# Kernel tuning notes

Measured on AMD Instinct MI355X. Metric: run time of the kernel, lower is better.

The kernel has to match this reference:

```python
import jax, jax.numpy as jnp
import numpy as np

N_HEADS = 16
MASK_FILL = -2.0**15 + 1.0  # -32767, matches torch reference


def setup_inputs() -> dict:
    key = jax.random.key(0)
    ks = jax.random.split(key, 10)
    B, N, D = 4, 2048, 1024
    sc = 0.02
    return {
        "q": jax.random.normal(ks[0], (B, N, D), jnp.float32),
        "k": jax.random.normal(ks[1], (B, N, D), jnp.float32),
        "v": jax.random.normal(ks[2], (B, N, D), jnp.float32),
        "Wq": jax.random.normal(ks[3], (D, D), jnp.float32) * sc,
        "bq": jnp.zeros((D,), jnp.float32),
        "Wk": jax.random.normal(ks[4], (D, D), jnp.float32) * sc,
        "bk": jnp.zeros((D,), jnp.float32),
        "Wv": jax.random.normal(ks[5], (D, D), jnp.float32) * sc,
        "bv": jnp.zeros((D,), jnp.float32),
        "Wo": jax.random.normal(ks[6], (D, D), jnp.float32) * sc,
    }


def reference(q, k, v, Wq, bq, Wk, bk, Wv, bv, Wo):
    B, N, D = q.shape
    H = N_HEADS
    dh = D // H
    scale = dh ** (-0.5)

    def proj(x, W, b):
        # torch nn.Linear: x @ W.T + b, W stored as (out, in)
        y = jnp.einsum('bnd,od->bno', x, W) + b
        return y.reshape(B, N, H, dh).transpose(0, 2, 1, 3)  # b h n d

    qh = proj(q, Wq, bq)
    kh = proj(k, Wk, bk)
    vh = proj(v, Wv, bv)

    scores = jnp.einsum('bhnd,bhmd->bhnm', qh, kh) * scale  # [B,H,N,N]
    causal = jnp.tril(jnp.ones((N, N), dtype=bool))
    scores = jnp.where(causal, scores, jnp.float32(MASK_FILL))
    attn = jax.nn.softmax(scores, axis=-1)
    x = jnp.einsum('bhnm,bhmd->bhnd', attn, vh)
    x = x.transpose(0, 2, 1, 3).reshape(B, N, D)  # b n (h d)
    return jnp.einsum('bnd,od->bno', x, Wo)  # to_out Linear, bias=False; dropout p=0
```

## Files before the change

### kernel.cpp

```cpp
#include <hip/hip_runtime.h>
#include <hip/hip_bf16.h>
#include <cstdint>
#include <cstddef>

typedef __bf16 bf16_t;
typedef __bf16 bf16x4 __attribute__((ext_vector_type(4)));
typedef __bf16 bf16x8 __attribute__((ext_vector_type(8)));
typedef float  f32x4  __attribute__((ext_vector_type(4)));

static constexpr int Bsz  = 4;
static constexpr int Nseq = 2048;
static constexpr int Dmod = 1024;
static constexpr int H    = 16;
static constexpr int DH   = 64;
static constexpr int M_TOT = Bsz * Nseq;
static constexpr int K    = 1024;
static constexpr int BM = 128, BN = 128, BK = 32;

#define WAITVM(N) asm volatile("s_waitcnt vmcnt(" #N ")" ::: "memory")

__device__ __forceinline__ f32x4 mfma16(bf16x8 a, bf16x8 b, f32x4 c) {
  return __builtin_amdgcn_mfma_f32_16x16x32_bf16(a, b, c, 0, 0, 0);
}

__device__ __forceinline__ bf16x8 cvt8(const float* p) {
  f32x4 lo = *(const f32x4*)(p);
  f32x4 hi = *(const f32x4*)(p + 4);
  bf16x8 r;
#pragma unroll
  for (int i = 0; i < 4; ++i) { r[i] = (bf16_t)lo[i]; r[4 + i] = (bf16_t)hi[i]; }
  return r;
}

__device__ __forceinline__ void async16(const bf16_t* g, bf16_t* l) {
  __builtin_amdgcn_global_load_lds(
      (const __attribute__((address_space(1))) void*)g,
      (__attribute__((address_space(3))) void*)l, 16, 0, 0);
}

struct CvtArgs {
  const float* src[7];
  bf16_t* dst[7];
  int n[7];
};

__global__ __launch_bounds__(256) void cvt_kernel(CvtArgs a) {
  const int z = blockIdx.y;
  const float* s = a.src[z];
  bf16x8* d = (bf16x8*)a.dst[z];
  const int n8 = a.n[z] >> 3;
  const int stride = gridDim.x * 256;
  for (int i = blockIdx.x * 256 + threadIdx.x; i < n8; i += stride)
    d[i] = cvt8(s + (size_t)i * 8);
}

template <int MODE, typename CT>
__device__ __forceinline__ void gemm_body(
    bf16_t (*As)[BM][BK], bf16_t (*Ws)[BN][BK],
    const bf16_t* __restrict__ A, const bf16_t* __restrict__ W,
    const float* __restrict__ bias, CT* __restrict__ C, float oscale) {
  const int tid  = threadIdx.x;
  const int lane = tid & 63;
  const int wave = tid >> 6;
  const int wm = wave & 1, wn = wave >> 1;
  const int row = lane & 15, quad = lane >> 4;

  const int m_blk = blockIdx.x * BM;
  const int n_blk = blockIdx.y * BN;

  f32x4 acc[4][4];
#pragma unroll
  for (int i = 0; i < 4; ++i)
#pragma unroll
    for (int j = 0; j < 4; ++j) acc[i][j] = (f32x4){0.f, 0.f, 0.f, 0.f};

  const int srow = lane >> 2;
  const int scol = (lane & 3) * 8;

  const bf16_t* Abase = A + (size_t)m_blk * K + scol;
  const bf16_t* Wbase = W + (size_t)n_blk * K + scol;

  constexpr int NT = K / BK;

  auto stage = [&](int t, int buf) {
#pragma unroll
    for (int j = 0; j < 2; ++j) {
      const int seg = wave * 2 + j;
      async16(Abase + (size_t)(seg * 16 + srow) * K + t * BK,
              &As[buf][seg * 16][0]);
      async16(Wbase + (size_t)(seg * 16 + srow) * K + t * BK,
              &Ws[buf][seg * 16][0]);
    }
  };

  stage(0, 0);
  stage(1, 1);
  int buf = 0, bufn = 2;

#pragma unroll 1
  for (int it = 0; it < NT; ++it) {
    if (it + 1 < NT) { WAITVM(4); } else { WAITVM(0); }
    __builtin_amdgcn_s_barrier();

    bf16x8 af[4], wf[4];
#pragma unroll
    for (int i = 0; i < 4; ++i)
      af[i] = *(const bf16x8*)(&As[buf][wm * 64 + i * 16 + row][quad * 8]);
#pragma unroll
    for (int i = 0; i < 4; ++i)
      wf[i] = *(const bf16x8*)(&Ws[buf][wn * 64 + i * 16 + row][quad * 8]);

    if (it + 2 < NT) stage(it + 2, bufn);

#pragma unroll
    for (int i = 0; i < 4; ++i)
#pragma unroll
      for (int j = 0; j < 4; ++j) {
        if (MODE == 1)
          acc[i][j] = mfma16(af[i], wf[j], acc[i][j]);
        else
          acc[i][j] = mfma16(wf[j], af[i], acc[i][j]);
      }

    buf  = (buf  == 2) ? 0 : buf  + 1;
    bufn = (bufn == 2) ? 0 : bufn + 1;
  }

  if (MODE == 0) {
#pragma unroll
    for (int i = 0; i < 4; ++i) {
      const int m = m_blk + wm * 64 + i * 16 + row;
      const int b = m >> 11, n = m & 2047;
#pragma unroll
      for (int j = 0; j < 4; ++j) {
        const int o0 = n_blk + wn * 64 + j * 16 + quad * 4;
        const int hh = o0 >> 6, od = o0 & 63;
        const f32x4 bv4 = *(const f32x4*)(bias + o0);
        const size_t idx0 = (((size_t)b * H + hh) * Nseq + n) * DH + od;
        bf16x4 pkt;
#pragma unroll
        for (int r = 0; r < 4; ++r)
          pkt[r] = (bf16_t)((acc[i][j][r] + bv4[r]) * oscale);
        *(bf16x4*)((bf16_t*)C + idx0) = pkt;
      }
    }
  } else if (MODE == 2) {
#pragma unroll
    for (int i = 0; i < 4; ++i) {
      const int m = m_blk + wm * 64 + i * 16 + row;
#pragma unroll
      for (int j = 0; j < 4; ++j) {
        const int o0 = n_blk + wn * 64 + j * 16 + quad * 4;
        *(f32x4*)((float*)C + (size_t)m * Dmod + o0) = acc[i][j];
      }
    }
  } else {
#pragma unroll
    for (int j = 0; j < 4; ++j) {
      const int o = n_blk + wn * 64 + j * 16 + row;
      const float bv = bias[o];
      const int hh = o >> 6, od = o & 63;
#pragma unroll
      for (int i = 0; i < 4; ++i) {
        const int m0 = m_blk + wm * 64 + i * 16 + quad * 4;
        const int b = m0 >> 11, n = m0 & 2047;
        const size_t idx0 = (((size_t)b * H + hh) * DH + od) * Nseq + n;
        bf16x4 pkt;
#pragma unroll
        for (int r = 0; r < 4; ++r)
          pkt[r] = (bf16_t)(acc[i][j][r] + bv);
        *(bf16x4*)((bf16_t*)C + idx0) = pkt;
      }
    }
  }
}

struct QkvArgs {
  const bf16_t* A[3];
  const bf16_t* W[3];
  const float*  bias[3];
  bf16_t*       out[3];
};

__global__ __launch_bounds__(256) void qkv_gemm(QkvArgs a, float qscale) {
  __shared__ bf16_t As[3][BM][BK];
  __shared__ bf16_t Ws[3][BN][BK];
  const int z = blockIdx.z;
  if (z == 2)
    gemm_body<1, bf16_t>(As, Ws, a.A[2], a.W[2], a.bias[2], a.out[2], 1.f);
  else if (z == 1)
    gemm_body<0, bf16_t>(As, Ws, a.A[1], a.W[1], a.bias[1], a.out[1], 1.f);
  else
    gemm_body<0, bf16_t>(As, Ws, a.A[0], a.W[0], a.bias[0], a.out[0], qscale);
}

__global__ __launch_bounds__(256) void out_gemm(
    const bf16_t* __restrict__ A, const bf16_t* __restrict__ W,
    float* __restrict__ C) {
  __shared__ bf16_t As[3][BM][BK];
  __shared__ bf16_t Ws[3][BN][BK];
  gemm_body<2, float>(As, Ws, A, W, nullptr, C, 1.f);
}

__global__ __launch_bounds__(256, 4) void attn_fwd(
    const bf16_t* __restrict__ Q, const bf16_t* __restrict__ Kh,
    const bf16_t* __restrict__ VT, bf16_t* __restrict__ X) {
  const int lane = threadIdx.x & 63;
  const int wave = threadIdx.x >> 6;
  const int bid = blockIdx.x;
  const int bh = (bid & 7) * 8 + ((bid >> 3) & 7);
  const int qt = 31 - (bid >> 6);
  const int b = bh >> 4, h = bh & 15;
  const int row = lane & 15, quad = lane >> 4;

  __shared__ __align__(16) bf16_t Kt[3][32][64];
  __shared__ __align__(16) bf16_t Vt[3][64][32];
  __shared__ __align__(16) bf16_t plds[4][16][56];

  const bf16_t* Qb = Q + (size_t)bh * Nseq * DH;
  const bf16_t* Kb = Kh + (size_t)bh * Nseq * DH;
  const bf16_t* Vb = VT + (size_t)bh * DH * Nseq;

  const int krow_l = lane >> 3;
  const int kc8    = lane & 7;
  const bf16_t* ksrc =
      Kb + (size_t)(wave * 8 + krow_l) * DH + (kc8 ^ krow_l) * 8;
  bf16_t* kdst = &Kt[0][wave * 8][0];

  const int vd_l = lane >> 2;
  const int vkc  = lane & 3;
  const int vd   = wave * 16 + vd_l;
  const bf16_t* vsrc =
      Vb + (size_t)vd * Nseq + (vkc ^ ((vd_l >> 1) & 3)) * 8;
  bf16_t* vdst = &Vt[0][wave * 16][0];

  auto stage = [&](int t, int buf) {
    async16(ksrc + (size_t)t * (32 * DH), kdst + buf * (32 * 64));
    async16(vsrc + t * 32, vdst + buf * (64 * 32));
  };

  const int q0 = qt * 64 + wave * 16;
  const int qg = q0 + row;

  bf16x8 qf0 = *(const bf16x8*)(Qb + (size_t)(q0 + row) * DH + quad * 8);
  bf16x8 qf1 = *(const bf16x8*)(Qb + (size_t)(q0 + row) * DH + 32 + quad * 8);

  f32x4 o_acc[4];
#pragma unroll
  for (int c = 0; c < 4; ++c) o_acc[c] = (f32x4){0.f, 0.f, 0.f, 0.f};
  f32x4 ls2[2];
  ls2[0] = (f32x4){0.f, 0.f, 0.f, 0.f};
  ls2[1] = (f32x4){0.f, 0.f, 0.f, 0.f};

  const int nfull = 2 * qt;
  const int NT = nfull + 2;

  stage(0, 0);
  stage(1, 1);
  int buf = 0, bufn = 2;

#pragma unroll 1
  for (int it = 0; it < NT; ++it) {
    if (it + 1 < NT) { WAITVM(2); } else { WAITVM(0); }
    __builtin_amdgcn_s_barrier();

    bf16x8 kf[2][2], vf[4];
#pragma unroll
    for (int c = 0; c < 2; ++c)
#pragma unroll
      for (int hf = 0; hf < 2; ++hf)
        kf[c][hf] = *(const bf16x8*)(
            &Kt[buf][c * 16 + row][((hf * 4 + quad) ^ (row & 7)) * 8]);
#pragma unroll
    for (int ch = 0; ch < 4; ++ch)
      vf[ch] = *(const bf16x8*)(
          &Vt[buf][ch * 16 + row][(quad ^ ((row >> 1) & 3)) * 8]);

    if (it + 2 < NT) stage(it + 2, bufn);

    f32x4 s[2];
    __builtin_amdgcn_s_setprio(1);
#pragma unroll
    for (int c = 0; c < 2; ++c) {
      s[c] = (f32x4){0.f, 0.f, 0.f, 0.f};
      s[c] = mfma16(kf[c][0], qf0, s[c]);
      s[c] = mfma16(kf[c][1], qf1, s[c]);
    }
    __builtin_amdgcn_s_setprio(0);

    const bool mask = (it >= nfull);
    const int k0 = it * 32;
#pragma unroll
    for (int c = 0; c < 2; ++c) {
      bf16x4 pk;
      f32x4 pv4;
#pragma unroll
      for (int r = 0; r < 4; ++r) {
        float t = s[c][r];
        if (mask) {
          const int kg = k0 + c * 16 + quad * 4 + r;
          t = (kg <= qg) ? t : -1e38f;
        }
        float pv = __builtin_amdgcn_exp2f(t);
        pv4[r] = pv;
        pk[r] = (bf16_t)pv;
      }
      ls2[c] += pv4;
      *(bf16x4*)(&plds[wave][row][c * 16 + quad * 4]) = pk;
    }
    __asm__ volatile("s_waitcnt lgkmcnt(0)" ::: "memory");
    const bf16x8 pf = *(const bf16x8*)(&plds[wave][row][quad * 8]);
    __builtin_amdgcn_s_setprio(1);
#pragma unroll
    for (int ch = 0; ch < 4; ++ch)
      o_acc[ch] = mfma16(pf, vf[ch], o_acc[ch]);
    __builtin_amdgcn_s_setprio(0);

    buf  = (buf  == 2) ? 0 : buf  + 1;
    bufn = (bufn == 2) ? 0 : bufn + 1;
  }

  float ls = (ls2[0][0] + ls2[0][1]) + (ls2[0][2] + ls2[0][3]) +
             (ls2[1][0] + ls2[1][1]) + (ls2[1][2] + ls2[1][3]);
  ls += __shfl_xor(ls, 16, 64);
  ls += __shfl_xor(ls, 32, 64);

#pragma unroll
  for (int r = 0; r < 4; ++r) {
    const float linv = 1.f / __shfl(ls, quad * 4 + r, 64);
    const int qq = q0 + quad * 4 + r;
    const size_t base = ((size_t)b * Nseq + qq) * Dmod + h * DH;
#pragma unroll
    for (int ch = 0; ch < 4; ++ch)
      X[base + ch * 16 + row] = (bf16_t)(o_acc[ch][r] * linv);
  }
}

extern "C" void kernel_launch(void* const* d_in, const int* in_sizes, int n_in,
                              void* d_out, int out_size, void* d_ws,
                              size_t ws_size, hipStream_t stream) {
  const float* q  = (const float*)d_in[0];
  const float* k  = (const float*)d_in[1];
  const float* v  = (const float*)d_in[2];
  const float* Wq = (const float*)d_in[3];
  const float* bq = (const float*)d_in[4];
  const float* Wk = (const float*)d_in[5];
  const float* bk = (const float*)d_in[6];
  const float* Wv = (const float*)d_in[7];
  const float* bv = (const float*)d_in[8];
  const float* Wo = (const float*)d_in[9];
  float* out = (float*)d_out;

  const size_t E  = (size_t)M_TOT * Dmod;
  const size_t EW = (size_t)Dmod * Dmod;
  bf16_t* ws = (bf16_t*)d_ws;
  bf16_t* qb  = ws;
  bf16_t* kb  = ws + E;
  bf16_t* vb  = ws + 2 * E;
  bf16_t* Wqb = ws + 3 * E;
  bf16_t* Wkb = Wqb + EW;
  bf16_t* Wvb = Wkb + EW;
  bf16_t* Wob = Wvb + EW;
  bf16_t* Qh  = Wob + EW;
  bf16_t* Kh  = Qh + E;
  bf16_t* VT  = Kh + E;
  bf16_t* X   = kb;

  CvtArgs ca;
  ca.src[0] = q;  ca.dst[0] = qb;  ca.n[0] = (int)E;
  ca.src[1] = k;  ca.dst[1] = kb;  ca.n[1] = (int)E;
  ca.src[2] = v;  ca.dst[2] = vb;  ca.n[2] = (int)E;
  ca.src[3] = Wq; ca.dst[3] = Wqb; ca.n[3] = (int)EW;
  ca.src[4] = Wk; ca.dst[4] = Wkb; ca.n[4] = (int)EW;
  ca.src[5] = Wv; ca.dst[5] = Wvb; ca.n[5] = (int)EW;
  ca.src[6] = Wo; ca.dst[6] = Wob; ca.n[6] = (int)EW;
  cvt_kernel<<<dim3(512, 7), 256, 0, stream>>>(ca);

  const float C_SC = 0.125f * 1.44269504088896f;

  dim3 blk(256);
  QkvArgs qa;
  qa.A[0] = qb; qa.W[0] = Wqb; qa.bias[0] = bq; qa.out[0] = Qh;
  qa.A[1] = kb; qa.W[1] = Wkb; qa.bias[1] = bk; qa.out[1] = Kh;
  qa.A[2] = vb; qa.W[2] = Wvb; qa.bias[2] = bv; qa.out[2] = VT;
  qkv_gemm<<<dim3(M_TOT / BM, Dmod / BN, 3), blk, 0, stream>>>(qa, C_SC);

  attn_fwd<<<dim3(2048), blk, 0, stream>>>(Qh, Kh, VT, X);

  out_gemm<<<dim3(M_TOT / BM, Dmod / BN), blk, 0, stream>>>(X, Wob, out);
}
```

Baseline: 317.1 us.

## Software-pipeline attention loop so PV of previous tile overlaps QK and softmax

Restructures the causal attention inner loop into a two-stage software pipeline, manually unrolled by two with ping-pong V-fragment and P-fragment registers. Each iteration issues the QK MFMAs for tile i together with the PV MFMAs for tile i-1 before doing the exp2 softmax for tile i. The goal is to hide MFMA latency behind the VALU softmax work and the LDS round trip for P. It also merges the two row-sum accumulators into one and replaces the explicit lgkmcnt wait with a compiler barrier. In exchange it needs more live registers, has longer prologue and epilogue code, and relies on the compiler inserting the LDS wait for the P write-then-read.

New measurement: 312.1 us. No clear change (-1.6%).

```diff
diff --git a/kernel.cpp b/kernel.cpp
--- a/kernel.cpp
+++ b/kernel.cpp
@@ -248,37 +248,26 @@
   f32x4 o_acc[4];
 #pragma unroll
   for (int c = 0; c < 4; ++c) o_acc[c] = (f32x4){0.f, 0.f, 0.f, 0.f};
-  f32x4 ls2[2];
-  ls2[0] = (f32x4){0.f, 0.f, 0.f, 0.f};
-  ls2[1] = (f32x4){0.f, 0.f, 0.f, 0.f};
+  f32x4 lsv = (f32x4){0.f, 0.f, 0.f, 0.f};
 
   const int nfull = 2 * qt;
   const int NT = nfull + 2;
 
-  stage(0, 0);
-  stage(1, 1);
-  int buf = 0, bufn = 2;
-
-#pragma unroll 1
-  for (int it = 0; it < NT; ++it) {
-    if (it + 1 < NT) { WAITVM(2); } else { WAITVM(0); }
-    __builtin_amdgcn_s_barrier();
-
-    bf16x8 kf[2][2], vf[4];
+  auto read_kf = [&](bf16x8 (&kf)[2][2], int bf) {
 #pragma unroll
     for (int c = 0; c < 2; ++c)
 #pragma unroll
       for (int hf = 0; hf < 2; ++hf)
         kf[c][hf] = *(const bf16x8*)(
-            &Kt[buf][c * 16 + row][((hf * 4 + quad) ^ (row & 7)) * 8]);
+            &Kt[bf][c * 16 + row][((hf * 4 + quad) ^ (row & 7)) * 8]);
+  };
+  auto read_vf = [&](bf16x8 (&vf)[4], int bf) {
 #pragma unroll
     for (int ch = 0; ch < 4; ++ch)
       vf[ch] = *(const bf16x8*)(
-          &Vt[buf][ch * 16 + row][(quad ^ ((row >> 1) & 3)) * 8]);
-
-    if (it + 2 < NT) stage(it + 2, bufn);
-
-    f32x4 s[2];
+          &Vt[bf][ch * 16 + row][(quad ^ ((row >> 1) & 3)) * 8]);
+  };
+  auto qk = [&](f32x4 (&s)[2], const bf16x8 (&kf)[2][2]) {
     __builtin_amdgcn_s_setprio(1);
 #pragma unroll
     for (int c = 0; c < 2; ++c) {
@@ -287,7 +276,15 @@
       s[c] = mfma16(kf[c][1], qf1, s[c]);
     }
     __builtin_amdgcn_s_setprio(0);
-
+  };
+  auto pv = [&](const bf16x8& pf, const bf16x8 (&vf)[4]) {
+    __builtin_amdgcn_s_setprio(1);
+#pragma unroll
+    for (int ch = 0; ch < 4; ++ch)
+      o_acc[ch] = mfma16(pf, vf[ch], o_acc[ch]);
+    __builtin_amdgcn_s_setprio(0);
+  };
+  auto softmax_store = [&](const f32x4 (&s)[2], int it, bf16x8& pfN) {
     const bool mask = (it >= nfull);
     const int k0 = it * 32;
 #pragma unroll
@@ -301,27 +298,82 @@
           const int kg = k0 + c * 16 + quad * 4 + r;
           t = (kg <= qg) ? t : -1e38f;
         }
-        float pv = __builtin_amdgcn_exp2f(t);
-        pv4[r] = pv;
-        pk[r] = (bf16_t)pv;
+        float p = __builtin_amdgcn_exp2f(t);
+        pv4[r] = p;
+        pk[r] = (bf16_t)p;
       }
-      ls2[c] += pv4;
+      lsv += pv4;
       *(bf16x4*)(&plds[wave][row][c * 16 + quad * 4]) = pk;
     }
-    __asm__ volatile("s_waitcnt lgkmcnt(0)" ::: "memory");
-    const bf16x8 pf = *(const bf16x8*)(&plds[wave][row][quad * 8]);
-    __builtin_amdgcn_s_setprio(1);
-#pragma unroll
-    for (int ch = 0; ch < 4; ++ch)
-      o_acc[ch] = mfma16(pf, vf[ch], o_acc[ch]);
-    __builtin_amdgcn_s_setprio(0);
-
-    buf  = (buf  == 2) ? 0 : buf  + 1;
-    bufn = (bufn == 2) ? 0 : bufn + 1;
-  }
-
-  float ls = (ls2[0][0] + ls2[0][1]) + (ls2[0][2] + ls2[0][3]) +
-             (ls2[1][0] + ls2[1][1]) + (ls2[1][2] + ls2[1][3]);
+    asm volatile("" ::: "memory");
+    pfN = *(const bf16x8*)(&plds[wave][row][quad * 8]);
+  };
+
+  bf16x8 vfA[4], vfB[4], pfA, pfB;
+
+  stage(0, 0);
+  stage(1, 1);
+
+  {
+    WAITVM(2);
+    __builtin_amdgcn_s_barrier();
+    bf16x8 kf[2][2];
+    read_kf(kf, 0);
+    read_vf(vfA, 0);
+    if (NT > 2) stage(2, 2);
+    f32x4 s[2];
+    qk(s, kf);
+    softmax_store(s, 0, pfA);
+  }
+
+  int buf = 1, bufn = (NT > 2) ? 0 : 2;
+
+#pragma unroll 1
+  for (int it = 1; it + 1 < NT; it += 2) {
+    {
+      WAITVM(2);
+      __builtin_amdgcn_s_barrier();
+      bf16x8 kf[2][2];
+      read_kf(kf, buf);
+      read_vf(vfB, buf);
+      if (it + 2 < NT) stage(it + 2, bufn);
+      f32x4 s[2];
+      qk(s, kf);
+      pv(pfA, vfA);
+      softmax_store(s, it, pfB);
+      buf  = (buf  == 2) ? 0 : buf  + 1;
+      bufn = (bufn == 2) ? 0 : bufn + 1;
+    }
+    {
+      WAITVM(2);
+      __builtin_amdgcn_s_barrier();
+      bf16x8 kf[2][2];
+      read_kf(kf, buf);
+      read_vf(vfA, buf);
+      if (it + 3 < NT) stage(it + 3, bufn);
+      f32x4 s[2];
+      qk(s, kf);
+      pv(pfB, vfB);
+      softmax_store(s, it + 1, pfA);
+      buf  = (buf  == 2) ? 0 : buf  + 1;
+      bufn = (bufn == 2) ? 0 : bufn + 1;
+    }
+  }
+
+  {
+    WAITVM(0);
+    __builtin_amdgcn_s_barrier();
+    bf16x8 kf[2][2];
+    read_kf(kf, buf);
+    read_vf(vfB, buf);
+    f32x4 s[2];
+    qk(s, kf);
+    pv(pfA, vfA);
+    softmax_store(s, NT - 1, pfB);
+  }
+  pv(pfB, vfB);
+
+  float ls = (lsv[0] + lsv[1]) + (lsv[2] + lsv[3]);
   ls += __shfl_xor(ls, 16, 64);
   ls += __shfl_xor(ls, 32, 64);
 
```
